# Performance work log

Measured on AMD Instinct MI355X. Metric: run time of the kernel, lower is better.

## Reference

```python
import jax, jax.numpy as jnp
import numpy as np

B, S, D = 2, 4096, 512
H = 8
W = 512            # local attention window size
HD = D // H        # head dim
NC = S // W        # number of chunks
HALF = W // 2      # symmetric half-window


def setup_inputs() -> dict:
    key = jax.random.key(0)
    ks = jax.random.split(key, 12)
    s = 1.0 / np.sqrt(D)
    return {
        "val": jax.random.normal(ks[0], (B, S, D), jnp.float32),
        "Wq": jax.random.normal(ks[1], (D, D), jnp.float32) * s,
        "bq": jnp.zeros((D,), jnp.float32),
        "Wk": jax.random.normal(ks[2], (D, D), jnp.float32) * s,
        "bk": jnp.zeros((D,), jnp.float32),
        "Wv": jax.random.normal(ks[3], (D, D), jnp.float32) * s,
        "bv": jnp.zeros((D,), jnp.float32),
        "Wo": jax.random.normal(ks[4], (D, D), jnp.float32) * s,
        "bo": jnp.zeros((D,), jnp.float32),
        "gamma": jnp.ones((D,), jnp.float32),
        "beta": jnp.zeros((D,), jnp.float32),
    }


def _heads(x):
    # [B,S,D] -> [B,H,S,HD]
    return x.reshape(B, S, H, HD).transpose(0, 2, 1, 3)


def _gather_neighbors(x):
    # x: [B,H,S,HD] -> [B,H,NC,3W,HD] (prev | cur | next chunk, zero-padded at ends)
    xp = jnp.pad(x, ((0, 0), (0, 0), (W, W), (0, 0)))
    xc = xp.reshape(B, H, NC + 2, W, HD)
    return jnp.concatenate([xc[:, :, :-2], xc[:, :, 1:-1], xc[:, :, 2:]], axis=3)


def _local_attention(x, Wq, bq, Wk, bk, Wv, bv, Wo, bo):
    q = _heads(x @ Wq + bq)
    k = _heads(x @ Wk + bk)
    v = _heads(x @ Wv + bv)

    qc = q.reshape(B, H, NC, W, HD)            # chunked queries
    kn = _gather_neighbors(k)                  # [B,H,NC,3W,HD]
    vn = _gather_neighbors(v)

    scale = 1.0 / np.sqrt(HD)
    scores = jnp.einsum("bhcqd,bhckd->bhcqk", qc, kn) * scale  # [B,H,NC,W,3W]

    # banded mask: key relative position in [-HALF, HALF], and key index in [0,S)
    qi = jnp.arange(W)[:, None]
    kj = jnp.arange(3 * W)[None, :]
    band = jnp.abs(kj - W - qi) <= HALF                          # [W,3W]
    key_pos = (jnp.arange(NC)[:, None, None] - 1) * W + kj[None]  # [NC,1,3W]
    valid = (key_pos >= 0) & (key_pos < S)                       # [NC,1,3W]
    mask = band[None] & valid                                    # [NC,W,3W]

    scores = jnp.where(mask[None, None], scores, jnp.float32(-1e9))
    p = jax.nn.softmax(scores, axis=-1)
    o = jnp.einsum("bhcqk,bhckd->bhcqd", p, vn)                  # [B,H,NC,W,HD]
    o = o.reshape(B, H, S, HD).transpose(0, 2, 1, 3).reshape(B, S, D)
    return o @ Wo + bo


def _layer_norm(x, gamma, beta, eps=1e-5):
    mu = jnp.mean(x, axis=-1, keepdims=True)
    var = jnp.mean(jnp.square(x - mu), axis=-1, keepdims=True)
    return (x - mu) * jax.lax.rsqrt(var + eps) * gamma + beta


def reference(val, Wq, bq, Wk, bk, Wv, bv, Wo, bo, gamma, beta):
    attn_out = _local_attention(val, Wq, bq, Wk, bk, Wv, bv, Wo, bo)
    return _layer_norm(val + attn_out, gamma, beta)
```

## Files before the change

### kernel.cpp

```cpp
#include <hip/hip_runtime.h>
#include <hip/hip_bf16.h>

#define BATCH 2
#define SEQ   4096
#define DIM   512
#define NHEAD 8
#define HDIM  64
#define ROWS  (BATCH*SEQ)

typedef float  fx4   __attribute__((ext_vector_type(4)));
typedef __bf16 bf16x8 __attribute__((ext_vector_type(8)));
typedef unsigned short ushort_t;
typedef unsigned short usx4 __attribute__((ext_vector_type(4)));
typedef unsigned short usx8 __attribute__((ext_vector_type(8)));

static __device__ __forceinline__ float b2f(ushort_t v) {
    union { unsigned int u; float f; } c; c.u = ((unsigned int)v) << 16; return c.f;
}
static __device__ __forceinline__ ushort_t f2b(float f) {
    union { float f; unsigned int u; } c; c.f = f;
    unsigned int u = c.u;
    unsigned int r = (u + 0x7FFFu + ((u >> 16) & 1u)) >> 16;
    return (ushort_t)r;
}
static __device__ __forceinline__ void gload16(const ushort_t* g, ushort_t* l) {
    __builtin_amdgcn_global_load_lds(
        (const __attribute__((address_space(1))) unsigned int*)g,
        (__attribute__((address_space(3))) unsigned int*)l, 16, 0, 0);
}

__global__ __launch_bounds__(256) void prep_kernel(
    const float* __restrict__ val, ushort_t* __restrict__ xb,
    const float* __restrict__ W0, const float* __restrict__ W1,
    const float* __restrict__ W2, const float* __restrict__ W3,
    ushort_t* __restrict__ T0, ushort_t* __restrict__ T1,
    ushort_t* __restrict__ T2, ushort_t* __restrict__ T3) {

    const int tid = threadIdx.x;
    if (blockIdx.y >= 4) {
        const int bid = blockIdx.x + 64 * (blockIdx.y - 4);
        const int stride = 256 * 256 * 4;
        for (int i = (bid * 256 + tid) * 4; i < ROWS * 512; i += stride) {
            fx4 v = *(const fx4*)(val + i);
            usx4 o; o.x = f2b(v.x); o.y = f2b(v.y); o.z = f2b(v.z); o.w = f2b(v.w);
            *(usx4*)(xb + i) = o;
        }
        return;
    }
    const float* W; ushort_t* WT;
    switch (blockIdx.y) {
        case 0: W = W0; WT = T0; break;
        case 1: W = W1; WT = T1; break;
        case 2: W = W2; WT = T2; break;
        default: W = W3; WT = T3; break;
    }
    __shared__ float tile[64][65];
    int r0 = (blockIdx.x & 7) * 64;
    int c0 = (blockIdx.x >> 3) * 64;
    for (int idx = tid; idx < 4096; idx += 256) {
        int rr = idx >> 6, cc = idx & 63;
        tile[rr][cc] = W[(c0 + rr) * 512 + (r0 + cc)];
    }
    __syncthreads();
    for (int idx = tid; idx < 4096; idx += 256) {
        int rr = idx >> 6, cc = idx & 63;
        WT[(size_t)(r0 + rr) * 512 + (c0 + cc)] = f2b(tile[cc][rr]);
    }
}

__global__ __launch_bounds__(256) void gemm128_kernel(
    const ushort_t* __restrict__ A,
    const ushort_t* __restrict__ BT0, const ushort_t* __restrict__ BT1, const ushort_t* __restrict__ BT2,
    const float* __restrict__ b0, const float* __restrict__ b1, const float* __restrict__ b2,
    ushort_t* __restrict__ C0, ushort_t* __restrict__ C1, ushort_t* __restrict__ C2) {

    const ushort_t* BT; const float* bias; ushort_t* C;
    if (blockIdx.z == 0)      { BT = BT0; bias = b0; C = C0; }
    else if (blockIdx.z == 1) { BT = BT1; bias = b1; C = C1; }
    else                      { BT = BT2; bias = b2; C = C2; }

    __shared__ ushort_t As[128 * 32];
    __shared__ ushort_t Bs[128 * 32];

    const int tid  = threadIdx.x;
    const int wave = tid >> 6;
    const int lane = tid & 63;
    const int lm   = lane & 15;
    const int quad = lane >> 4;
    const int wm   = wave >> 1;
    const int wn   = wave & 1;

    const int m0t = blockIdx.x * 128;
    const int n0t = blockIdx.y * 128;

    const int srow = tid >> 2, sgc = tid & 3;
    const ushort_t* ga0 = A  + (size_t)(m0t + srow) * 512 + sgc * 8;
    const ushort_t* ga1 = ga0 + (size_t)64 * 512;
    const ushort_t* gb0 = BT + (size_t)(n0t + srow) * 512 + sgc * 8;
    const ushort_t* gb1 = gb0 + (size_t)64 * 512;
    ushort_t* la0 = As + tid * 8;
    ushort_t* la1 = As + (tid + 256) * 8;
    ushort_t* lb0 = Bs + tid * 8;
    ushort_t* lb1 = Bs + (tid + 256) * 8;

    const int aoff = (wm * 64 + lm) * 32 + quad * 8;
    const int boff = (wn * 64 + lm) * 32 + quad * 8;

    fx4 acc[4][4];
    #pragma unroll
    for (int i = 0; i < 4; ++i)
        #pragma unroll
        for (int j = 0; j < 4; ++j) acc[i][j] = 0;

    for (int k0 = 0; k0 < 512; k0 += 32) {
        __syncthreads();
        gload16(ga0 + k0, la0);
        gload16(ga1 + k0, la1);
        gload16(gb0 + k0, lb0);
        gload16(gb1 + k0, lb1);
        __syncthreads();

        bf16x8 af[4], bfr[4];
        #pragma unroll
        for (int ms = 0; ms < 4; ++ms) af[ms]  = *(const bf16x8*)&As[aoff + ms * 512];
        #pragma unroll
        for (int ns = 0; ns < 4; ++ns) bfr[ns] = *(const bf16x8*)&Bs[boff + ns * 512];
        #pragma unroll
        for (int ms = 0; ms < 4; ++ms)
            #pragma unroll
            for (int ns = 0; ns < 4; ++ns)
                acc[ms][ns] = __builtin_amdgcn_mfma_f32_16x16x32_bf16(af[ms], bfr[ns], acc[ms][ns], 0, 0, 0);
    }

    const int crow0 = m0t + wm * 64 + quad * 4;
    const int ccol0 = n0t + wn * 64 + lm;

    if (blockIdx.z == 2) {
        #pragma unroll
        for (int ns = 0; ns < 4; ++ns) {
            int col = ccol0 + ns * 16;
            int h = col >> 6, d = col & 63;
            float bv = bias[col];
            #pragma unroll
            for (int ms = 0; ms < 4; ++ms) {
                int m = crow0 + ms * 16;
                int bb = m >> 12, s0 = m & 4095;
                usx4 o;
                o.x = f2b(acc[ms][ns][0] + bv); o.y = f2b(acc[ms][ns][1] + bv);
                o.z = f2b(acc[ms][ns][2] + bv); o.w = f2b(acc[ms][ns][3] + bv);
                *(usx4*)(C + (((size_t)(bb * 8 + h) * 64 + d) * 4096 + s0)) = o;
            }
        }
    } else {
        #pragma unroll
        for (int ns = 0; ns < 4; ++ns) {
            int col = ccol0 + ns * 16;
            float bv = bias[col];
            #pragma unroll
            for (int ms = 0; ms < 4; ++ms) {
                #pragma unroll
                for (int r = 0; r < 4; ++r) {
                    C[(size_t)(crow0 + ms * 16 + r) * 512 + col] = f2b(acc[ms][ns][r] + bv);
                }
            }
        }
    }
}

__global__ __launch_bounds__(256, 4) void attn_mfma_kernel(
    const ushort_t* __restrict__ Qb, const ushort_t* __restrict__ Kb,
    const ushort_t* __restrict__ Vt, ushort_t* __restrict__ Ob) {

    __shared__ ushort_t Klds[64 * 64];
    __shared__ ushort_t Vlds[64 * 64];
    __shared__ ushort_t Plds[4 * 16 * 72];

    const int tid  = threadIdx.x;
    const int wave = tid >> 6;
    const int lane = tid & 63;
    const int lm   = lane & 15;
    const int quad = lane >> 4;

    const int bh = blockIdx.y;
    const int b = bh >> 3, h = bh & 7;
    const int q0 = blockIdx.x * 64;
    const int qw = q0 + wave * 16;

    const ushort_t* qp = Qb + ((size_t)(b * SEQ + qw + lm)) * 512 + h * 64 + quad * 8;
    bf16x8 qf0 = *(const bf16x8*)qp;
    bf16x8 qf1 = *(const bf16x8*)(qp + 32);

    int koff[2][4], voff[2][4];
    #pragma unroll
    for (int ks = 0; ks < 2; ++ks) {
        #pragma unroll
        for (int tn = 0; tn < 4; ++tn) {
            int key = tn * 16 + lm;
            koff[ks][tn] = key * 64 + (((ks * 4 + quad) ^ (key & 7)) * 8);
            int d = tn * 16 + lm;
            voff[ks][tn] = d * 64 + (((ks * 4 + quad) ^ (d & 7)) * 8);
        }
    }
    ushort_t* Pw = Plds + wave * (16 * 72);
    const int pwbase = lm * 72 + quad * 4;
    const int prbase = lm * 72 + quad * 8;

    const int skey = tid >> 3;
    const int sdg  = tid & 7;
    const size_t kgbase = ((size_t)b * SEQ) * 512 + h * 64 + sdg * 8;
    const size_t vgbase = ((size_t)bh * 64) * 4096 + sdg * 8;
    const int l0 = skey * 64 + ((sdg ^ (skey & 7)) * 8);
    const int l1 = l0 + 32 * 64;

    const int klo = (q0 >= 256) ? 0 : ((256 - q0) >> 6);
    const int khi = min(8, (4288 - q0) >> 6);

    bf16x8 onesf;
    {
        __bf16 o = (lm == 0) ? (__bf16)1.0f : (__bf16)0.0f;
        #pragma unroll
        for (int j = 0; j < 8; ++j) onesf[j] = o;
    }

    fx4 oacc[4];
    oacc[0] = 0; oacc[1] = 0; oacc[2] = 0; oacc[3] = 0;
    fx4 lacc = 0;

    usx8 kn0, kn1, vn0, vn1;
    {
        int ts = q0 - 256 + klo * 64;
        kn0 = *(const usx8*)(Kb + kgbase + (size_t)(ts + skey) * 512);
        kn1 = *(const usx8*)(Kb + kgbase + (size_t)(ts + skey + 32) * 512);
        vn0 = *(const usx8*)(Vt + vgbase + (size_t)skey * 4096 + ts);
        vn1 = *(const usx8*)(Vt + vgbase + (size_t)(skey + 32) * 4096 + ts);
    }

    for (int kt = klo; kt <= khi; ++kt) {
        const int ts = q0 - 256 + kt * 64;
        __syncthreads();
        *(usx8*)&Klds[l0] = kn0;
        *(usx8*)&Klds[l1] = kn1;
        *(usx8*)&Vlds[l0] = vn0;
        *(usx8*)&Vlds[l1] = vn1;
        __syncthreads();

        if (kt < khi) {
            int t2 = ts + 64;
            kn0 = *(const usx8*)(Kb + kgbase + (size_t)(t2 + skey) * 512);
            kn1 = *(const usx8*)(Kb + kgbase + (size_t)(t2 + skey + 32) * 512);
            vn0 = *(const usx8*)(Vt + vgbase + (size_t)skey * 4096 + t2);
            vn1 = *(const usx8*)(Vt + vgbase + (size_t)(skey + 32) * 4096 + t2);
        }

        bf16x8 kf[2][4];
        #pragma unroll
        for (int ks = 0; ks < 2; ++ks)
            #pragma unroll
            for (int tn = 0; tn < 4; ++tn)
                kf[ks][tn] = *(const bf16x8*)&Klds[koff[ks][tn]];
        fx4 sacc[4];
        sacc[0] = 0; sacc[1] = 0; sacc[2] = 0; sacc[3] = 0;
        #pragma unroll
        for (int ks = 0; ks < 2; ++ks) {
            bf16x8 q8 = ks ? qf1 : qf0;
            #pragma unroll
            for (int tn = 0; tn < 4; ++tn)
                sacc[tn] = __builtin_amdgcn_mfma_f32_16x16x32_bf16(kf[ks][tn], q8, sacc[tn], 0, 0, 0);
        }

        const bool edge = (ts < qw - 241) || (ts > qw + 193);
        const int qg = qw + lm;
        #pragma unroll
        for (int tn = 0; tn < 4; ++tn) {
            usx4 pk;
            #pragma unroll
            for (int r = 0; r < 4; ++r) {
                float p = __expf(sacc[tn][r] * 0.125f);
                if (edge) {
                    int dlt = (ts + tn * 16 + quad * 4 + r) - qg;
                    p = (dlt <= 256 && dlt >= -256) ? p : 0.0f;
                }
                pk[r] = f2b(p);
            }
            *(usx4*)&Pw[pwbase + tn * 16] = pk;
        }

        bf16x8 vf[2][4];
        #pragma unroll
        for (int ks = 0; ks < 2; ++ks)
            #pragma unroll
            for (int tn = 0; tn < 4; ++tn)
                vf[ks][tn] = *(const bf16x8*)&Vlds[voff[ks][tn]];
        #pragma unroll
        for (int ks = 0; ks < 2; ++ks) {
            bf16x8 ap = *(const bf16x8*)&Pw[prbase + ks * 32];
            lacc = __builtin_amdgcn_mfma_f32_16x16x32_bf16(ap, onesf, lacc, 0, 0, 0);
            #pragma unroll
            for (int tn = 0; tn < 4; ++tn)
                oacc[tn] = __builtin_amdgcn_mfma_f32_16x16x32_bf16(ap, vf[ks][tn], oacc[tn], 0, 0, 0);
        }
    }

    float linv[4];
    #pragma unroll
    for (int r = 0; r < 4; ++r) {
        float lv = __shfl(lacc[r], (lane & 48));
        linv[r] = 1.0f / lv;
    }
    ushort_t* ob = Ob + ((size_t)(b * SEQ + qw + quad * 4)) * 512 + h * 64 + lm;
    #pragma unroll
    for (int tn = 0; tn < 4; ++tn)
        #pragma unroll
        for (int r = 0; r < 4; ++r)
            ob[(size_t)r * 512 + tn * 16] = f2b(oacc[tn][r] * linv[r]);
}

__global__ __launch_bounds__(256) void ln_kernel(
    const ushort_t* __restrict__ xb, const ushort_t* __restrict__ ob,
    const float* __restrict__ gamma, const float* __restrict__ beta,
    float* __restrict__ out) {

    int row  = blockIdx.x * 4 + (threadIdx.x >> 6);
    int lane = threadIdx.x & 63;

    const ushort_t* xp = xb + (size_t)row * 512 + lane * 8;
    const ushort_t* op = ob + (size_t)row * 512 + lane * 8;

    usx4 xa = ((const usx4*)xp)[0];
    usx4 xc = ((const usx4*)xp)[1];
    usx4 oa = ((const usx4*)op)[0];
    usx4 oc = ((const usx4*)op)[1];
    fx4 va, vb;
    va.x = b2f(xa.x) + b2f(oa.x); va.y = b2f(xa.y) + b2f(oa.y);
    va.z = b2f(xa.z) + b2f(oa.z); va.w = b2f(xa.w) + b2f(oa.w);
    vb.x = b2f(xc.x) + b2f(oc.x); vb.y = b2f(xc.y) + b2f(oc.y);
    vb.z = b2f(xc.z) + b2f(oc.z); vb.w = b2f(xc.w) + b2f(oc.w);

    float s = va.x + va.y + va.z + va.w + vb.x + vb.y + vb.z + vb.w;
    #pragma unroll
    for (int m = 32; m > 0; m >>= 1) s += __shfl_xor(s, m);
    float mu = s * (1.0f / 512.0f);

    fx4 da = va - mu;
    fx4 db = vb - mu;
    float ss = da.x*da.x + da.y*da.y + da.z*da.z + da.w*da.w
             + db.x*db.x + db.y*db.y + db.z*db.z + db.w*db.w;
    #pragma unroll
    for (int m = 32; m > 0; m >>= 1) ss += __shfl_xor(ss, m);
    float rstd = rsqrtf(ss * (1.0f / 512.0f) + 1e-5f);

    const fx4* gp = (const fx4*)(gamma + lane * 8);
    const fx4* bp = (const fx4*)(beta  + lane * 8);
    fx4 g0 = gp[0], g1 = gp[1], b0 = bp[0], b1 = bp[1];

    float* outp = out + (size_t)row * 512 + lane * 8;
    fx4 r0 = da * rstd * g0 + b0;
    fx4 r1 = db * rstd * g1 + b1;
    ((fx4*)outp)[0] = r0;
    ((fx4*)outp)[1] = r1;
}

extern "C" void kernel_launch(void* const* d_in, const int* in_sizes, int n_in,
                              void* d_out, int out_size, void* d_ws, size_t ws_size,
                              hipStream_t stream) {
    const float* val   = (const float*)d_in[0];
    const float* Wq    = (const float*)d_in[1];
    const float* bq    = (const float*)d_in[2];
    const float* Wk    = (const float*)d_in[3];
    const float* bk    = (const float*)d_in[4];
    const float* Wv    = (const float*)d_in[5];
    const float* bv    = (const float*)d_in[6];
    const float* Wo    = (const float*)d_in[7];
    const float* bo    = (const float*)d_in[8];
    const float* gamma = (const float*)d_in[9];
    const float* beta  = (const float*)d_in[10];
    float* out = (float*)d_out;

    char* w = (char*)d_ws;
    ushort_t* xb    = (ushort_t*)w; w += (size_t)ROWS * 512 * 2;
    ushort_t* WqT   = (ushort_t*)w; w += 512 * 512 * 2;
    ushort_t* WkT   = (ushort_t*)w; w += 512 * 512 * 2;
    ushort_t* WvT   = (ushort_t*)w; w += 512 * 512 * 2;
    ushort_t* WoT   = (ushort_t*)w; w += 512 * 512 * 2;
    ushort_t* Qb    = (ushort_t*)w; w += (size_t)ROWS * 512 * 2;
    ushort_t* Kb    = (ushort_t*)w; w += (size_t)ROWS * 512 * 2;
    ushort_t* Vtb   = (ushort_t*)w; w += (size_t)ROWS * 512 * 2;
    ushort_t* attnb = (ushort_t*)w; w += (size_t)ROWS * 512 * 2;
    ushort_t* obuf  = (ushort_t*)w; w += (size_t)ROWS * 512 * 2;

    prep_kernel<<<dim3(64, 8), 256, 0, stream>>>(
        val, xb, Wq, Wk, Wv, Wo, WqT, WkT, WvT, WoT);

    gemm128_kernel<<<dim3(ROWS / 128, 4, 3), 256, 0, stream>>>(
        xb, WqT, WkT, WvT, bq, bk, bv, Qb, Kb, Vtb);

    attn_mfma_kernel<<<dim3(SEQ / 64, BATCH * NHEAD), 256, 0, stream>>>(Qb, Kb, Vtb, attnb);

    gemm128_kernel<<<dim3(ROWS / 128, 4, 1), 256, 0, stream>>>(
        attnb, WoT, WoT, WoT, bo, bo, bo, obuf, obuf, obuf);

    ln_kernel<<<ROWS / 4, 256, 0, stream>>>(xb, obuf, gamma, beta, out);
}
```

Before: 165.3 us.

## Split attention key tiles across wave pairs and use narrower output GEMM tiles

The attention kernel now gives each wave 32 queries (two 16-row groups) instead of 16. Wave pairs alternate key tiles, and the partial outputs and row sums are combined through shared memory at the end. This lets each K fragment loaded from LDS feed two query groups, which cuts LDS read traffic per MFMA. The cost is idle half-iterations per wave, a larger shared-memory footprint, and an extra reduction step. Separately, the output projection uses a new 128x64-tile GEMM with twice as many blocks, to improve occupancy and CU coverage for the single-matrix GEMM.

```diff
diff --git a/kernel.cpp b/kernel.cpp
--- a/kernel.cpp
+++ b/kernel.cpp
@@ -167,28 +167,99 @@
     }
 }
 
-__global__ __launch_bounds__(256, 4) void attn_mfma_kernel(
-    const ushort_t* __restrict__ Qb, const ushort_t* __restrict__ Kb,
-    const ushort_t* __restrict__ Vt, ushort_t* __restrict__ Ob) {
-
-    __shared__ ushort_t Klds[64 * 64];
-    __shared__ ushort_t Vlds[64 * 64];
-    __shared__ ushort_t Plds[4 * 16 * 72];
+__global__ __launch_bounds__(256) void gemm_n64_kernel(
+    const ushort_t* __restrict__ A, const ushort_t* __restrict__ BT,
+    const float* __restrict__ bias, ushort_t* __restrict__ C) {
+
+    __shared__ ushort_t As[128 * 32];
+    __shared__ ushort_t Bs[64 * 32];
 
     const int tid  = threadIdx.x;
     const int wave = tid >> 6;
     const int lane = tid & 63;
     const int lm   = lane & 15;
     const int quad = lane >> 4;
+    const int wm   = wave >> 1;
+    const int wn   = wave & 1;
+
+    const int m0t = blockIdx.x * 128;
+    const int n0t = blockIdx.y * 64;
+
+    const int srow = tid >> 2, sgc = tid & 3;
+    const ushort_t* ga0 = A  + (size_t)(m0t + srow) * 512 + sgc * 8;
+    const ushort_t* ga1 = ga0 + (size_t)64 * 512;
+    const ushort_t* gb  = BT + (size_t)(n0t + srow) * 512 + sgc * 8;
+
+    const int aoff = (wm * 64 + lm) * 32 + quad * 8;
+    const int boff = (wn * 32 + lm) * 32 + quad * 8;
+
+    fx4 acc[4][2];
+    #pragma unroll
+    for (int i = 0; i < 4; ++i) { acc[i][0] = 0; acc[i][1] = 0; }
+
+    for (int k0 = 0; k0 < 512; k0 += 32) {
+        __syncthreads();
+        gload16(ga0 + k0, As + tid * 8);
+        gload16(ga1 + k0, As + (tid + 256) * 8);
+        gload16(gb + k0, Bs + tid * 8);
+        __syncthreads();
+
+        bf16x8 af[4], bfr[2];
+        #pragma unroll
+        for (int ms = 0; ms < 4; ++ms) af[ms]  = *(const bf16x8*)&As[aoff + ms * 512];
+        #pragma unroll
+        for (int ns = 0; ns < 2; ++ns) bfr[ns] = *(const bf16x8*)&Bs[boff + ns * 512];
+        #pragma unroll
+        for (int ms = 0; ms < 4; ++ms)
+            #pragma unroll
+            for (int ns = 0; ns < 2; ++ns)
+                acc[ms][ns] = __builtin_amdgcn_mfma_f32_16x16x32_bf16(af[ms], bfr[ns], acc[ms][ns], 0, 0, 0);
+    }
+
+    const int crow0 = m0t + wm * 64 + quad * 4;
+    const int ccol0 = n0t + wn * 32 + lm;
+    #pragma unroll
+    for (int ns = 0; ns < 2; ++ns) {
+        int col = ccol0 + ns * 16;
+        float bv = bias[col];
+        #pragma unroll
+        for (int ms = 0; ms < 4; ++ms)
+            #pragma unroll
+            for (int r = 0; r < 4; ++r)
+                C[(size_t)(crow0 + ms * 16 + r) * 512 + col] = f2b(acc[ms][ns][r] + bv);
+    }
+}
+
+__global__ __launch_bounds__(256, 4) void attn_mfma_kernel(
+    const ushort_t* __restrict__ Qb, const ushort_t* __restrict__ Kb,
+    const ushort_t* __restrict__ Vt, ushort_t* __restrict__ Ob) {
+
+    __shared__ __align__(16) char smem[16384 + 18432];
+    ushort_t* Klds = (ushort_t*)smem;
+    ushort_t* Vlds = (ushort_t*)(smem + 8192);
+
+    const int tid  = threadIdx.x;
+    const int wave = tid >> 6;
+    const int lane = tid & 63;
+    const int lm   = lane & 15;
+    const int quad = lane >> 4;
+    const int qh   = wave & 1;
+    const int tp   = wave >> 1;
 
     const int bh = blockIdx.y;
     const int b = bh >> 3, h = bh & 7;
     const int q0 = blockIdx.x * 64;
-    const int qw = q0 + wave * 16;
-
-    const ushort_t* qp = Qb + ((size_t)(b * SEQ + qw + lm)) * 512 + h * 64 + quad * 8;
-    bf16x8 qf0 = *(const bf16x8*)qp;
-    bf16x8 qf1 = *(const bf16x8*)(qp + 32);
+    const int qw = q0 + qh * 32;
+
+    ushort_t* Pw = (ushort_t*)(smem + 16384) + wave * 2304;
+
+    bf16x8 qf[2][2];
+    #pragma unroll
+    for (int qg = 0; qg < 2; ++qg) {
+        const ushort_t* qp = Qb + ((size_t)(b * SEQ + qw + qg * 16 + lm)) * 512 + h * 64 + quad * 8;
+        qf[qg][0] = *(const bf16x8*)qp;
+        qf[qg][1] = *(const bf16x8*)(qp + 32);
+    }
 
     int koff[2][4], voff[2][4];
     #pragma unroll
@@ -201,9 +272,6 @@
             voff[ks][tn] = d * 64 + (((ks * 4 + quad) ^ (d & 7)) * 8);
         }
     }
-    ushort_t* Pw = Plds + wave * (16 * 72);
-    const int pwbase = lm * 72 + quad * 4;
-    const int prbase = lm * 72 + quad * 8;
 
     const int skey = tid >> 3;
     const int sdg  = tid & 7;
@@ -222,9 +290,13 @@
         for (int j = 0; j < 8; ++j) onesf[j] = o;
     }
 
-    fx4 oacc[4];
-    oacc[0] = 0; oacc[1] = 0; oacc[2] = 0; oacc[3] = 0;
-    fx4 lacc = 0;
+    fx4 oacc[2][4];
+    #pragma unroll
+    for (int qg = 0; qg < 2; ++qg)
+        #pragma unroll
+        for (int tn = 0; tn < 4; ++tn) oacc[qg][tn] = 0;
+    fx4 lacc[2];
+    lacc[0] = 0; lacc[1] = 0;
 
     usx8 kn0, kn1, vn0, vn1;
     {
@@ -252,37 +324,43 @@
             vn1 = *(const usx8*)(Vt + vgbase + (size_t)(skey + 32) * 4096 + t2);
         }
 
+        if ((kt & 1) != tp) continue;
+
         bf16x8 kf[2][4];
         #pragma unroll
         for (int ks = 0; ks < 2; ++ks)
             #pragma unroll
             for (int tn = 0; tn < 4; ++tn)
                 kf[ks][tn] = *(const bf16x8*)&Klds[koff[ks][tn]];
-        fx4 sacc[4];
-        sacc[0] = 0; sacc[1] = 0; sacc[2] = 0; sacc[3] = 0;
-        #pragma unroll
-        for (int ks = 0; ks < 2; ++ks) {
-            bf16x8 q8 = ks ? qf1 : qf0;
-            #pragma unroll
-            for (int tn = 0; tn < 4; ++tn)
-                sacc[tn] = __builtin_amdgcn_mfma_f32_16x16x32_bf16(kf[ks][tn], q8, sacc[tn], 0, 0, 0);
-        }
-
-        const bool edge = (ts < qw - 241) || (ts > qw + 193);
-        const int qg = qw + lm;
-        #pragma unroll
-        for (int tn = 0; tn < 4; ++tn) {
-            usx4 pk;
-            #pragma unroll
-            for (int r = 0; r < 4; ++r) {
-                float p = __expf(sacc[tn][r] * 0.125f);
-                if (edge) {
-                    int dlt = (ts + tn * 16 + quad * 4 + r) - qg;
-                    p = (dlt <= 256 && dlt >= -256) ? p : 0.0f;
+
+        #pragma unroll
+        for (int qg = 0; qg < 2; ++qg) {
+            fx4 sacc[4];
+            sacc[0] = 0; sacc[1] = 0; sacc[2] = 0; sacc[3] = 0;
+            #pragma unroll
+            for (int ks = 0; ks < 2; ++ks) {
+                bf16x8 q8 = qf[qg][ks];
+                #pragma unroll
+                for (int tn = 0; tn < 4; ++tn)
+                    sacc[tn] = __builtin_amdgcn_mfma_f32_16x16x32_bf16(kf[ks][tn], q8, sacc[tn], 0, 0, 0);
+            }
+            const int qbase = qw + qg * 16;
+            const bool edge = (ts < qbase - 241) || (ts > qbase + 193);
+            const int qg_q = qbase + lm;
+            #pragma unroll
+            for (int tn = 0; tn < 4; ++tn) {
+                usx4 pk;
+                #pragma unroll
+                for (int r = 0; r < 4; ++r) {
+                    float p = __expf(sacc[tn][r] * 0.125f);
+                    if (edge) {
+                        int dlt = (ts + tn * 16 + quad * 4 + r) - qg_q;
+                        p = (dlt <= 256 && dlt >= -256) ? p : 0.0f;
+                    }
+                    pk[r] = f2b(p);
                 }
-                pk[r] = f2b(p);
+                *(usx4*)&Pw[(qg * 16 + lm) * 72 + tn * 16 + quad * 4] = pk;
             }
-            *(usx4*)&Pw[pwbase + tn * 16] = pk;
         }
 
         bf16x8 vf[2][4];
@@ -292,27 +370,58 @@
             for (int tn = 0; tn < 4; ++tn)
                 vf[ks][tn] = *(const bf16x8*)&Vlds[voff[ks][tn]];
         #pragma unroll
-        for (int ks = 0; ks < 2; ++ks) {
-            bf16x8 ap = *(const bf16x8*)&Pw[prbase + ks * 32];
-            lacc = __builtin_amdgcn_mfma_f32_16x16x32_bf16(ap, onesf, lacc, 0, 0, 0);
+        for (int qg = 0; qg < 2; ++qg) {
+            #pragma unroll
+            for (int ks = 0; ks < 2; ++ks) {
+                bf16x8 ap = *(const bf16x8*)&Pw[(qg * 16 + lm) * 72 + ks * 32 + quad * 8];
+                lacc[qg] = __builtin_amdgcn_mfma_f32_16x16x32_bf16(ap, onesf, lacc[qg], 0, 0, 0);
+                #pragma unroll
+                for (int tn = 0; tn < 4; ++tn)
+                    oacc[qg][tn] = __builtin_amdgcn_mfma_f32_16x16x32_bf16(ap, vf[ks][tn], oacc[qg][tn], 0, 0, 0);
+            }
+        }
+    }
+
+    __syncthreads();
+    float* Ocomb = (float*)smem;
+    float* Lcomb = (float*)(smem + 17408);
+    if (tp == 1) {
+        #pragma unroll
+        for (int qg = 0; qg < 2; ++qg) {
             #pragma unroll
             for (int tn = 0; tn < 4; ++tn)
-                oacc[tn] = __builtin_amdgcn_mfma_f32_16x16x32_bf16(ap, vf[ks][tn], oacc[tn], 0, 0, 0);
-        }
-    }
-
-    float linv[4];
-    #pragma unroll
-    for (int r = 0; r < 4; ++r) {
-        float lv = __shfl(lacc[r], (lane & 48));
-        linv[r] = 1.0f / lv;
-    }
-    ushort_t* ob = Ob + ((size_t)(b * SEQ + qw + quad * 4)) * 512 + h * 64 + lm;
-    #pragma unroll
-    for (int tn = 0; tn < 4; ++tn)
-        #pragma unroll
-        for (int r = 0; r < 4; ++r)
-            ob[(size_t)r * 512 + tn * 16] = f2b(oacc[tn][r] * linv[r]);
+                #pragma unroll
+                for (int r = 0; r < 4; ++r)
+                    Ocomb[qh * 2176 + (qg * 16 + quad * 4 + r) * 68 + tn * 16 + lm] = oacc[qg][tn][r];
+        }
+        if (lm == 0) {
+            #pragma unroll
+            for (int qg = 0; qg < 2; ++qg)
+                #pragma unroll
+                for (int r = 0; r < 4; ++r)
+                    Lcomb[qh * 32 + qg * 16 + quad * 4 + r] = lacc[qg][r];
+        }
+    }
+    __syncthreads();
+    if (tp == 0) {
+        #pragma unroll
+        for (int qg = 0; qg < 2; ++qg) {
+            float linv[4];
+            #pragma unroll
+            for (int r = 0; r < 4; ++r) {
+                float lv = __shfl(lacc[qg][r], (lane & 48)) + Lcomb[qh * 32 + qg * 16 + quad * 4 + r];
+                linv[r] = 1.0f / lv;
+            }
+            ushort_t* ob = Ob + ((size_t)(b * SEQ + qw + qg * 16 + quad * 4)) * 512 + h * 64 + lm;
+            #pragma unroll
+            for (int tn = 0; tn < 4; ++tn)
+                #pragma unroll
+                for (int r = 0; r < 4; ++r) {
+                    float v = oacc[qg][tn][r] + Ocomb[qh * 2176 + (qg * 16 + quad * 4 + r) * 68 + tn * 16 + lm];
+                    ob[(size_t)r * 512 + tn * 16] = f2b(v * linv[r]);
+                }
+        }
+    }
 }
 
 __global__ __launch_bounds__(256) void ln_kernel(
@@ -396,8 +505,7 @@
 
     attn_mfma_kernel<<<dim3(SEQ / 64, BATCH * NHEAD), 256, 0, stream>>>(Qb, Kb, Vtb, attnb);
 
-    gemm128_kernel<<<dim3(ROWS / 128, 4, 1), 256, 0, stream>>>(
-        attnb, WoT, WoT, WoT, bo, bo, bo, obuf, obuf, obuf);
+    gemm_n64_kernel<<<dim3(ROWS / 128, 8), 256, 0, stream>>>(attnb, WoT, bo, obuf);
 
     ln_kernel<<<ROWS / 4, 256, 0, stream>>>(xb, obuf, gamma, beta, out);
 }
```

Result: slower. 187.6 us (+13.5%).
